# Kernel optimization log

Hardware: AMD Instinct MI355X
Metric: run time of the kernel (lower is better)

## Reference

```python
import jax, jax.numpy as jnp
import numpy as np

DIM=2048; NH=16; QK_NOPE=128; QK_ROPE=64; QK_HD=QK_NOPE+QK_ROPE; V_HD=128
Q_LORA=1536; KV_LORA=512
IDX_NH=16; IDX_HD=128; IDX_TOPK=1024
B=1; S=2048
NEG=-1e30  # finite stand-in for -inf mask

def _hadamard(n):
    H=np.array([[1.0]],dtype=np.float32)
    while H.shape[0]<n:
        H=np.block([[H,H],[H,-H]])
    return H
_H=jnp.asarray(_hadamard(IDX_HD),jnp.bfloat16)  # symmetric Sylvester Hadamard

def _rope_tables(s,d):
    inv=1.0/(10000.0**(np.arange(0,d,2)/float(d)))
    ang=np.outer(np.arange(s),inv)
    return jnp.asarray(np.cos(ang),jnp.float32),jnp.asarray(np.sin(ang),jnp.float32)

def _rope_interleaved(x,cos,sin):
    # pairs (x[2i], x[2i+1]); x: (b,s,h,d), cos/sin: (s,d//2)
    x1=x[...,0::2]; x2=x[...,1::2]
    c=cos[None,:,None,:]; s_=sin[None,:,None,:]
    return jnp.stack([x1*c-x2*s_,x1*s_+x2*c],axis=-1).reshape(x.shape)

def _rope_half(x,cos,sin):
    # non-interleaved: pairs (x[i], x[i+d/2])
    d=x.shape[-1]//2
    x1=x[...,:d]; x2=x[...,d:]
    c=cos[None,:,None,:]; s_=sin[None,:,None,:]
    return jnp.concatenate([x1*c-x2*s_,x1*s_+x2*c],axis=-1)

def _rms(x,w,eps=1e-6):
    xf=x.astype(jnp.float32)
    xf=xf*jax.lax.rsqrt(jnp.mean(xf*xf,axis=-1,keepdims=True)+eps)
    return (w*xf).astype(x.dtype)

def _ln(x,w,b,eps=1e-6):
    xf=x.astype(jnp.float32)
    mu=jnp.mean(xf,axis=-1,keepdims=True)
    var=jnp.mean((xf-mu)**2,axis=-1,keepdims=True)
    return ((xf-mu)*jax.lax.rsqrt(var+eps)*w+b).astype(x.dtype)

def _rotate(x):
    # rotate_activation: bf16 Hadamard transform, x @ H * d^-0.5 (H symmetric)
    return (x.astype(jnp.bfloat16)@_H)*(IDX_HD**-0.5)

def _forward(x,start_pos,freqs_cos,freqs_sin,mask,q_a_proj,q_a_ln_w,q_b_proj,kv_a_proj,kv_a_ln_w,kv_b_proj,o_proj,idx_wq_b,idx_wk,idx_knorm_w,idx_knorm_b,idx_weights_proj):
    b,s,_=x.shape  # start_pos==0 prefill -> cache slice == current k/kv
    sm_scale=QK_HD**-0.5
    qr=_rms(x@q_a_proj.T,q_a_ln_w)                       # (b,s,q_lora)
    q=(qr@q_b_proj.T).reshape(b,s,NH,QK_HD)
    q_nope=q[...,:QK_NOPE]
    q_pe=_rope_interleaved(q[...,QK_NOPE:],freqs_cos,freqs_sin)
    kvp=x@kv_a_proj.T
    kv=_rms(kvp[...,:KV_LORA],kv_a_ln_w)                 # latent kv cache (b,t,c)
    k_pe=_rope_interleaved(kvp[...,KV_LORA:][:,:,None,:],freqs_cos,freqs_sin)[:,:,0,:]
    # ---------- Indexer ----------
    iq=(qr@idx_wq_b.T).reshape(b,s,IDX_NH,IDX_HD)
    iq=jnp.concatenate([_rope_half(iq[...,:QK_ROPE],freqs_cos,freqs_sin),iq[...,QK_ROPE:]],axis=-1)
    ik=_ln(x@idx_wk.T,idx_knorm_w,idx_knorm_b)           # (b,s,IDX_HD)
    ik=jnp.concatenate([_rope_half(ik[:,:,None,:QK_ROPE],freqs_cos,freqs_sin)[:,:,0,:],ik[...,QK_ROPE:]],axis=-1)
    iq=_rotate(iq); ik=_rotate(ik)                       # bf16 Hadamard-rotated
    iw=(x@idx_weights_proj.T)*(IDX_NH**-0.5)             # (b,s,hI)
    wq=(iw[...,None]*iq.astype(jnp.float32)*(IDX_HD**-0.5)).astype(jnp.bfloat16)
    sc=jnp.einsum('bshd,btd->bsht',wq,ik,preferred_element_type=jnp.float32)
    index_score=jax.nn.relu(sc).sum(axis=2)+mask[None]   # bf16_index: relu, head-sum
    _,topk=jax.lax.top_k(index_score,min(IDX_TOPK,s))    # (b,s,K)
    imask=jnp.full((b,s,s),jnp.float32(NEG))
    imask=imask.at[jnp.arange(b)[:,None,None],jnp.arange(s)[None,:,None],topk].set(0.0)
    imask=imask+mask[None]
    # ---------- Latent attention (absorbed) ----------
    wkv=kv_b_proj.reshape(NH,QK_NOPE+V_HD,KV_LORA)
    q_abs=jnp.einsum('bshd,hdc->bshc',q_nope,wkv[:,:QK_NOPE])
    scores=(jnp.einsum('bshc,btc->bsht',q_abs,kv)+jnp.einsum('bshr,btr->bsht',q_pe,k_pe))*sm_scale
    scores=scores+imask[:,:,None,:]
    p=jax.nn.softmax(scores.astype(jnp.float32),axis=-1).astype(x.dtype)
    o=jnp.einsum('bsht,btc->bshc',p,kv)
    o=jnp.einsum('bshc,hdc->bshd',o,wkv[:,QK_NOPE:])
    return o.reshape(b,s,NH*V_HD)@o_proj.T

def setup_inputs():
    key=jax.random.key(0)
    ks=jax.random.split(key,10)
    def w(k,shape):
        return jax.random.normal(k,shape,jnp.float32)*(shape[-1]**-0.5)
    cos,sin=_rope_tables(S,QK_ROPE)
    causal=jnp.where(jnp.triu(jnp.ones((S,S),bool),1),jnp.float32(NEG),jnp.float32(0.0))
    return {
        'x':jax.random.normal(ks[0],(B,S,DIM),jnp.float32),
        'start_pos':0,
        'freqs_cos':cos,'freqs_sin':sin,'mask':causal,
        'q_a_proj':w(ks[1],(Q_LORA,DIM)),
        'q_a_ln_w':jnp.ones((Q_LORA,),jnp.float32),
        'q_b_proj':w(ks[2],(NH*QK_HD,Q_LORA)),
        'kv_a_proj':w(ks[3],(KV_LORA+QK_ROPE,DIM)),
        'kv_a_ln_w':jnp.ones((KV_LORA,),jnp.float32),
        'kv_b_proj':w(ks[4],(NH*(QK_NOPE+V_HD),KV_LORA)),
        'o_proj':w(ks[5],(DIM,NH*V_HD)),
        'idx_wq_b':w(ks[6],(IDX_NH*IDX_HD,Q_LORA)),
        'idx_wk':w(ks[7],(IDX_HD,DIM)),
        'idx_knorm_w':jnp.ones((IDX_HD,),jnp.float32),
        'idx_knorm_b':jnp.zeros((IDX_HD,),jnp.float32),
        'idx_weights_proj':w(ks[8],(IDX_NH,DIM)),
    }

def reference(x,start_pos,freqs_cos,freqs_sin,mask,q_a_proj,q_a_ln_w,q_b_proj,kv_a_proj,kv_a_ln_w,kv_b_proj,o_proj,idx_wq_b,idx_wk,idx_knorm_w,idx_knorm_b,idx_weights_proj):
    return _forward(x,start_pos,freqs_cos,freqs_sin,mask,q_a_proj,q_a_ln_w,q_b_proj,kv_a_proj,kv_a_ln_w,kv_b_proj,o_proj,idx_wq_b,idx_wk,idx_knorm_w,idx_knorm_b,idx_weights_proj)
```

## Files before the change

### kernel.cpp

```cpp
#include <hip/hip_runtime.h>
#include <hip/hip_bf16.h>
#include <math.h>

#define S 2048
#define NH 16
#define DIM 2048
#define QK_NOPE 128
#define QK_ROPE 64
#define QK_HD 192
#define V_HD 128
#define Q_LORA 1536
#define KV_LORA 512
#define IDX_HD 128
#define SM_SCALE 0.07216878364870323f
#define SCHUNK 512
#define PADK 40
#define XPLD 2256
#define QLD 5120
#define XPLD_PAD 2304

typedef __hip_bfloat16 bf16;
typedef unsigned short ushort_t;
typedef __attribute__((ext_vector_type(8))) short short8;
typedef __attribute__((ext_vector_type(4))) float f32x4;

__device__ __forceinline__ f32x4 mfma_bf16(short8 a, short8 b, f32x4 c) {
    return __builtin_amdgcn_mfma_f32_16x16x32_bf16(a, b, c, 0, 0, 0);
}
__device__ __forceinline__ void async16(const void* g, void* l) {
    __builtin_amdgcn_global_load_lds((const __attribute__((address_space(1))) void*)g,
                                     (__attribute__((address_space(3))) void*)l, 16, 0, 0);
}
__device__ __forceinline__ unsigned short f2bf(float f) {
    unsigned int u = __float_as_uint(f);
    return (unsigned short)((u + 0x7fff + ((u >> 16) & 1)) >> 16);
}
__device__ __forceinline__ float bf2f(unsigned short b) {
    return __uint_as_float(((unsigned int)b) << 16);
}

__global__ __launch_bounds__(256) void split_kernel(const float* __restrict__ in, ushort_t* __restrict__ hi,
                                                    ushort_t* __restrict__ lo, int n4) {
    int idx = blockIdx.x * 256 + threadIdx.x;
    if (idx >= n4) return;
    float4 v = ((const float4*)in)[idx];
    ushort4 h, l;
    h.x = f2bf(v.x); l.x = f2bf(v.x - bf2f(h.x));
    h.y = f2bf(v.y); l.y = f2bf(v.y - bf2f(h.y));
    h.z = f2bf(v.z); l.z = f2bf(v.z - bf2f(h.z));
    h.w = f2bf(v.w); l.w = f2bf(v.w - bf2f(h.w));
    ((ushort4*)hi)[idx] = h;
    ((ushort4*)lo)[idx] = l;
}

__global__ __launch_bounds__(256) void splitw2_kernel(const float* __restrict__ kv_b,
                                                      ushort_t* __restrict__ w2h, ushort_t* __restrict__ w2l) {
    int idx = blockIdx.x * 256 + threadIdx.x;
    int h = idx >> 14, rem = idx & 16383;
    int row = rem >> 7, c4 = (rem & 127) * 4;
    float4 v = *(const float4*)(kv_b + ((size_t)(h * 256 + 128 + row)) * 512 + c4);
    ushort4 hh, ll;
    hh.x = f2bf(v.x); ll.x = f2bf(v.x - bf2f(hh.x));
    hh.y = f2bf(v.y); ll.y = f2bf(v.y - bf2f(hh.y));
    hh.z = f2bf(v.z); ll.z = f2bf(v.z - bf2f(hh.z));
    hh.w = f2bf(v.w); ll.w = f2bf(v.w - bf2f(hh.w));
    *(ushort4*)(w2h + ((size_t)(h * 128 + row)) * 512 + c4) = hh;
    *(ushort4*)(w2l + ((size_t)(h * 128 + row)) * 512 + c4) = ll;
}

__global__ __launch_bounds__(256) void gemm3_lds(const ushort_t* __restrict__ Ah, const ushort_t* __restrict__ Al,
                                                 const ushort_t* __restrict__ Bh, const ushort_t* __restrict__ Bl,
                                                 float* __restrict__ C, int M, int N, int K) {
    __shared__ ushort_t sAh[128 * 32], sAl[128 * 32], sBh[128 * 32], sBl[128 * 32];
    const int tid = threadIdx.x;
    const int bm = blockIdx.y * 128, bn = blockIdx.x * 128;
    const int w = tid >> 6, lane = tid & 63;
    const int wm = (w >> 1) * 64, wn = (w & 1) * 64;
    const int fr = lane & 15, fk = (lane >> 4) * 8;
    const int srow = tid >> 2, skc = (tid & 3) * 8;
    f32x4 acc[4][4];
    for (int i = 0; i < 4; ++i)
        for (int j = 0; j < 4; ++j) acc[i][j] = f32x4{0.f, 0.f, 0.f, 0.f};
    const ushort_t* pAh0 = Ah + (size_t)(bm + srow) * K + skc;
    const ushort_t* pAh1 = Ah + (size_t)(bm + 64 + srow) * K + skc;
    const ushort_t* pAl0 = Al + (size_t)(bm + srow) * K + skc;
    const ushort_t* pAl1 = Al + (size_t)(bm + 64 + srow) * K + skc;
    const ushort_t* pBh0 = Bh + (size_t)(bn + srow) * K + skc;
    const ushort_t* pBh1 = Bh + (size_t)(bn + 64 + srow) * K + skc;
    const ushort_t* pBl0 = Bl + (size_t)(bn + srow) * K + skc;
    const ushort_t* pBl1 = Bl + (size_t)(bn + 64 + srow) * K + skc;
    ushort_t* dA0 = &sAh[srow * 32 + skc];
    ushort_t* dA1 = &sAh[(64 + srow) * 32 + skc];
    ushort_t* dAl0 = &sAl[srow * 32 + skc];
    ushort_t* dAl1 = &sAl[(64 + srow) * 32 + skc];
    ushort_t* dB0 = &sBh[srow * 32 + skc];
    ushort_t* dB1 = &sBh[(64 + srow) * 32 + skc];
    ushort_t* dBl0 = &sBl[srow * 32 + skc];
    ushort_t* dBl1 = &sBl[(64 + srow) * 32 + skc];
    for (int k0 = 0; k0 < K; k0 += 32) {
        __syncthreads();
        async16(pAh0, dA0);  async16(pAh1, dA1);
        async16(pAl0, dAl0); async16(pAl1, dAl1);
        async16(pBh0, dB0);  async16(pBh1, dB1);
        async16(pBl0, dBl0); async16(pBl1, dBl1);
        pAh0 += 32; pAh1 += 32; pAl0 += 32; pAl1 += 32;
        pBh0 += 32; pBh1 += 32; pBl0 += 32; pBl1 += 32;
        __syncthreads();
        short8 ahf[4], alf[4], bhf[4], blf[4];
        for (int i = 0; i < 4; ++i) {
            int ro = (wm + i * 16 + fr) * 32 + fk;
            ahf[i] = *(const short8*)&sAh[ro];
            alf[i] = *(const short8*)&sAl[ro];
        }
        for (int j = 0; j < 4; ++j) {
            int ro = (wn + j * 16 + fr) * 32 + fk;
            bhf[j] = *(const short8*)&sBh[ro];
            blf[j] = *(const short8*)&sBl[ro];
        }
        for (int i = 0; i < 4; ++i)
            for (int j = 0; j < 4; ++j) {
                acc[i][j] = mfma_bf16(ahf[i], bhf[j], acc[i][j]);
                acc[i][j] = mfma_bf16(ahf[i], blf[j], acc[i][j]);
                acc[i][j] = mfma_bf16(alf[i], bhf[j], acc[i][j]);
            }
    }
    const int cr = (lane >> 4) * 4, cc = lane & 15;
    for (int i = 0; i < 4; ++i)
        for (int j = 0; j < 4; ++j) {
            int row = bm + wm + i * 16 + cr;
            int col = bn + wn + j * 16 + cc;
            if (col < N)
                for (int r = 0; r < 4; ++r)
                    C[(size_t)(row + r) * N + col] = acc[i][j][r];
        }
}

__global__ __launch_bounds__(256) void rms_kernel(const float* __restrict__ in, float* __restrict__ out,
                                                  const float* __restrict__ w, int C, int ldin, int ldout) {
    const int row = blockIdx.x;
    const float* xr = in + (size_t)row * ldin;
    float* yr = out + (size_t)row * ldout;
    float ss = 0.f;
    for (int c = threadIdx.x; c < C; c += 256) { float v = xr[c]; ss += v * v; }
    for (int o = 32; o; o >>= 1) ss += __shfl_down(ss, o, 64);
    __shared__ float red[4];
    const int wave = threadIdx.x >> 6, lane = threadIdx.x & 63;
    if (lane == 0) red[wave] = ss;
    __syncthreads();
    const float tot = red[0] + red[1] + red[2] + red[3];
    const float scale = rsqrtf(tot / (float)C + 1e-6f);
    for (int c = threadIdx.x; c < C; c += 256) yr[c] = w[c] * (xr[c] * scale);
}

__global__ __launch_bounds__(256) void rms_split_kernel(const float* __restrict__ in, ushort_t* __restrict__ hi,
                                                        ushort_t* __restrict__ lo, const float* __restrict__ w,
                                                        int C, int ldin) {
    const int row = blockIdx.x;
    const float* xr = in + (size_t)row * ldin;
    float ss = 0.f;
    for (int c = threadIdx.x; c < C; c += 256) { float v = xr[c]; ss += v * v; }
    for (int o = 32; o; o >>= 1) ss += __shfl_down(ss, o, 64);
    __shared__ float red[4];
    const int wave = threadIdx.x >> 6, lane = threadIdx.x & 63;
    if (lane == 0) red[wave] = ss;
    __syncthreads();
    const float tot = red[0] + red[1] + red[2] + red[3];
    const float scale = rsqrtf(tot / (float)C + 1e-6f);
    for (int c = threadIdx.x; c < C; c += 256) {
        float v = w[c] * (xr[c] * scale);
        unsigned short h = f2bf(v);
        hi[(size_t)row * C + c] = h;
        lo[(size_t)row * C + c] = f2bf(v - bf2f(h));
    }
}

__global__ __launch_bounds__(128) void ln_kernel(float* __restrict__ x, const float* __restrict__ w,
                                                 const float* __restrict__ b, int ld) {
    const int row = blockIdx.x;
    float* xr = x + (size_t)row * ld;
    const int tid = threadIdx.x;
    float v = xr[tid];
    float sm = v;
    for (int o = 32; o; o >>= 1) sm += __shfl_down(sm, o, 64);
    __shared__ float red[2];
    if ((tid & 63) == 0) red[tid >> 6] = sm;
    __syncthreads();
    const float mu = (red[0] + red[1]) * (1.f / 128.f);
    __syncthreads();
    float d = v - mu;
    float sv = d * d;
    for (int o = 32; o; o >>= 1) sv += __shfl_down(sv, o, 64);
    if ((tid & 63) == 0) red[tid >> 6] = sv;
    __syncthreads();
    const float var = (red[0] + red[1]) * (1.f / 128.f);
    const float rs = rsqrtf(var + 1e-6f);
    xr[tid] = (v - mu) * rs * w[tid] + b[tid];
}

__global__ __launch_bounds__(256) void rope_inter_kernel(float* __restrict__ X, const float* __restrict__ ct,
                                                         const float* __restrict__ st, int H, int hs, int off,
                                                         int ld) {
    int idx = blockIdx.x * 256 + threadIdx.x;
    int k = idx & 31;
    int h = (idx >> 5) % H;
    int s = idx / (32 * H);
    if (s >= S) return;
    float c = ct[s * 32 + k], sn = st[s * 32 + k];
    float* p = X + (size_t)s * ld + h * hs + off;
    float x1 = p[2 * k], x2 = p[2 * k + 1];
    p[2 * k]     = x1 * c - x2 * sn;
    p[2 * k + 1] = x1 * sn + x2 * c;
}

__global__ __launch_bounds__(256) void rope_half_kernel(float* __restrict__ X, const float* __restrict__ ct,
                                                        const float* __restrict__ st, int H, int hs, int ld) {
    int idx = blockIdx.x * 256 + threadIdx.x;
    int k = idx & 31;
    int h = (idx >> 5) % H;
    int s = idx / (32 * H);
    if (s >= S) return;
    float c = ct[s * 32 + k], sn = st[s * 32 + k];
    float* p = X + (size_t)s * ld + h * hs;
    float x1 = p[k], x2 = p[32 + k];
    p[k]      = x1 * c - x2 * sn;
    p[32 + k] = x1 * sn + x2 * c;
}

__global__ __launch_bounds__(128) void rotate_kernel(const float* __restrict__ in, int lds, int H,
                                                     bf16* __restrict__ out) {
    __shared__ float xs[128];
    const int r = blockIdx.x, j = threadIdx.x;
    const int s = r / H, h = r - s * H;
    float v = in[(size_t)s * lds + h * 128 + j];
    xs[j] = __bfloat162float(__float2bfloat16(v));
    __syncthreads();
    float acc = 0.f;
    for (int d = 0; d < 128; ++d) {
        float xv = xs[d];
        acc += (__popc(d & j) & 1) ? -xv : xv;
    }
    float t = __bfloat162float(__float2bfloat16(acc)) * 0.08838834764831845f;
    out[(size_t)r * 128 + j] = __float2bfloat16(t);
}

__global__ __launch_bounds__(256) void wq_kernel(const float* __restrict__ iwb, bf16* __restrict__ iqr) {
    int idx = blockIdx.x * 256 + threadIdx.x;
    int s = idx >> 11, h = (idx >> 7) & 15;
    float a = 0.25f * iwb[(size_t)s * XPLD + h];
    float v = __bfloat162float(iqr[idx]);
    float t = (a * v) * 0.08838834764831845f;
    iqr[idx] = __float2bfloat16(t);
}

__global__ __launch_bounds__(256) void iscore_mfma(const bf16* __restrict__ wq, const bf16* __restrict__ ik,
                                                   float* __restrict__ out) {
    if (blockIdx.x > blockIdx.y) return;
    __shared__ unsigned short As[128 * 32], Bs[128 * 32];
    const int bs = blockIdx.y * 128, bt = blockIdx.x * 128;
    const int tid = threadIdx.x, w = tid >> 6, lane = tid & 63;
    const int wm = (w >> 1) * 64, wn = (w & 1) * 64;
    const int fr = lane & 15, fk = (lane >> 4) * 8;
    const int srow = lane >> 2, skc = (lane & 3) * 8;
    f32x4 sum[4][4];
    for (int i = 0; i < 4; ++i)
        for (int j = 0; j < 4; ++j) sum[i][j] = f32x4{0.f, 0.f, 0.f, 0.f};
    for (int h = 0; h < 16; ++h) {
        f32x4 acc[4][4];
        for (int i = 0; i < 4; ++i)
            for (int j = 0; j < 4; ++j) acc[i][j] = f32x4{0.f, 0.f, 0.f, 0.f};
        for (int k0 = 0; k0 < 128; k0 += 32) {
            __syncthreads();
            for (int i = 0; i < 2; ++i) {
                int seg = i * 4 + w;
                async16(wq + (size_t)(bs + seg * 16 + srow) * 2048 + h * 128 + k0 + skc, &As[seg * 512]);
                async16(ik + (size_t)(bt + seg * 16 + srow) * 128 + k0 + skc, &Bs[seg * 512]);
            }
            __syncthreads();
            short8 af[4], bff[4];
            for (int i = 0; i < 4; ++i) af[i]  = *(const short8*)&As[(wm + i * 16 + fr) * 32 + fk];
            for (int j = 0; j < 4; ++j) bff[j] = *(const short8*)&Bs[(wn + j * 16 + fr) * 32 + fk];
            for (int i = 0; i < 4; ++i)
                for (int j = 0; j < 4; ++j)
                    acc[i][j] = mfma_bf16(af[i], bff[j], acc[i][j]);
        }
        for (int i = 0; i < 4; ++i)
            for (int j = 0; j < 4; ++j)
                for (int r = 0; r < 4; ++r)
                    sum[i][j][r] += fmaxf(acc[i][j][r], 0.f);
    }
    const int cr = (lane >> 4) * 4, cc = lane & 15;
    for (int i = 0; i < 4; ++i)
        for (int j = 0; j < 4; ++j)
            for (int r = 0; r < 4; ++r)
                out[(size_t)(bs + wm + i * 16 + cr + r) * 2048 + bt + wn + j * 16 + cc] = sum[i][j][r];
}

__global__ __launch_bounds__(256) void topk_kernel(const float* __restrict__ isc, int* __restrict__ tk) {
    __shared__ unsigned long long keys[2048];
    const int s = blockIdx.x;
    const float* row = isc + (size_t)s * 2048;
    for (int t = threadIdx.x; t < 2048; t += 256) {
        unsigned long long kk = 0ull;
        if (t <= s) {
            unsigned int vb = __float_as_uint(row[t]);
            kk = ((unsigned long long)vb << 32) | (unsigned int)(2048 - t);
        }
        keys[t] = kk;
    }
    __syncthreads();
    for (int k = 2; k <= 2048; k <<= 1) {
        for (int j = k >> 1; j > 0; j >>= 1) {
            for (int t = threadIdx.x; t < 2048; t += 256) {
                int l = t ^ j;
                if (l > t) {
                    bool up = ((t & k) == 0);
                    unsigned long long a = keys[t], b = keys[l];
                    bool sw = up ? (a < b) : (a > b);
                    if (sw) { keys[t] = b; keys[l] = a; }
                }
            }
            __syncthreads();
        }
    }
    const int cnt = min(1024, s + 1);
    for (int i = threadIdx.x; i < 1024; i += 256) {
        int t = (i < cnt) ? (2048 - (int)(keys[i] & 0xFFFFFFFFull)) : -1;
        tk[(size_t)s * 1024 + i] = t;
    }
}

__global__ __launch_bounds__(256) void w1t_kernel(const float* __restrict__ kv_b, float* __restrict__ w1t) {
    __shared__ float ts[64][65];
    const int cb = blockIdx.x * 64, db = blockIdx.y * 64, h = blockIdx.z;
    const int t = threadIdx.x;
    for (int it = 0; it < 16; ++it) {
        int idx = it * 256 + t;
        int rr = idx >> 6, cc = idx & 63;
        ts[rr][cc] = kv_b[(size_t)(h * 256 + db + rr) * 512 + cb + cc];
    }
    __syncthreads();
    for (int it = 0; it < 16; ++it) {
        int idx = it * 256 + t;
        int rr = idx >> 6, cc = idx & 63;
        w1t[(size_t)h * 65536 + (size_t)(cb + rr) * 128 + db + cc] = ts[cc][rr];
    }
}

__global__ __launch_bounds__(576) void kvsplit_kernel(const float* __restrict__ kv, const float* __restrict__ kpe,
                                                      ushort_t* __restrict__ kvh, ushort_t* __restrict__ kvl,
                                                      unsigned int* __restrict__ kvi) {
    const int t = blockIdx.x, c = threadIdx.x;
    float v = (c < 512) ? kv[(size_t)t * 512 + c] : kpe[(size_t)t * XPLD + c];
    unsigned short hi = f2bf(v);
    unsigned short lo = f2bf(v - bf2f(hi));
    kvh[(size_t)t * 576 + c] = hi;
    kvl[(size_t)t * 576 + c] = lo;
    if (c < 512) kvi[(size_t)t * 512 + c] = (unsigned int)hi | ((unsigned int)lo << 16);
}

__global__ __launch_bounds__(256) void qabs_mfma(const float* __restrict__ q, const float* __restrict__ w1t,
                                                 ushort_t* __restrict__ qah, ushort_t* __restrict__ qal) {
    __shared__ unsigned short Ah[128 * PADK], Al[128 * PADK], Bh[128 * PADK], Bl[128 * PADK];
    const int tid = threadIdx.x;
    const int bn = blockIdx.x * 128, bm = blockIdx.y * 128, h = blockIdx.z;
    const int w = tid >> 6, lane = tid & 63;
    const int wm = (w >> 1) * 64, wn = (w & 1) * 64;
    const int fr = lane & 15, fk = (lane >> 4) * 8;
    f32x4 acc[4][4];
    for (int i = 0; i < 4; ++i)
        for (int j = 0; j < 4; ++j) acc[i][j] = f32x4{0.f, 0.f, 0.f, 0.f};
    for (int k0 = 0; k0 < 128; k0 += 32) {
        __syncthreads();
        for (int it = 0; it < 4; ++it) {
            int f = it * 256 + tid;
            int row = f >> 3, kc = (f & 7) * 4;
            float4 av = *(const float4*)(q + (size_t)(bm + row) * QLD + h * QK_HD + k0 + kc);
            float4 bv = *(const float4*)(w1t + (size_t)h * 65536 + (size_t)(bn + row) * 128 + k0 + kc);
            ushort4 ahi, alo, bhi, blo;
            ahi.x = f2bf(av.x); alo.x = f2bf(av.x - bf2f(ahi.x));
            ahi.y = f2bf(av.y); alo.y = f2bf(av.y - bf2f(ahi.y));
            ahi.z = f2bf(av.z); alo.z = f2bf(av.z - bf2f(ahi.z));
            ahi.w = f2bf(av.w); alo.w = f2bf(av.w - bf2f(ahi.w));
            bhi.x = f2bf(bv.x); blo.x = f2bf(bv.x - bf2f(bhi.x));
            bhi.y = f2bf(bv.y); blo.y = f2bf(bv.y - bf2f(bhi.y));
            bhi.z = f2bf(bv.z); blo.z = f2bf(bv.z - bf2f(bhi.z));
            bhi.w = f2bf(bv.w); blo.w = f2bf(bv.w - bf2f(bhi.w));
            *(ushort4*)&Ah[row * PADK + kc] = ahi;
            *(ushort4*)&Al[row * PADK + kc] = alo;
            *(ushort4*)&Bh[row * PADK + kc] = bhi;
            *(ushort4*)&Bl[row * PADK + kc] = blo;
        }
        __syncthreads();
        short8 ahf[4], alf[4], bhf[4], blf[4];
        for (int i = 0; i < 4; ++i) {
            int ro = (wm + i * 16 + fr) * PADK + fk;
            ahf[i] = *(const short8*)&Ah[ro];
            alf[i] = *(const short8*)&Al[ro];
        }
        for (int j = 0; j < 4; ++j) {
            int ro = (wn + j * 16 + fr) * PADK + fk;
            bhf[j] = *(const short8*)&Bh[ro];
            blf[j] = *(const short8*)&Bl[ro];
        }
        for (int i = 0; i < 4; ++i)
            for (int j = 0; j < 4; ++j) {
                acc[i][j] = mfma_bf16(ahf[i], bhf[j], acc[i][j]);
                acc[i][j] = mfma_bf16(ahf[i], blf[j], acc[i][j]);
                acc[i][j] = mfma_bf16(alf[i], bhf[j], acc[i][j]);
            }
    }
    const int cr = (lane >> 4) * 4, cc = lane & 15;
    for (int i = 0; i < 4; ++i)
        for (int j = 0; j < 4; ++j)
            for (int r = 0; r < 4; ++r) {
                int srow = bm + wm + i * 16 + cr + r;
                int col = bn + wn + j * 16 + cc;
                float f = acc[i][j][r] * SM_SCALE;
                size_t addr = ((size_t)srow * 16 + h) * 576 + col;
                unsigned short hi = f2bf(f);
                qah[addr] = hi;
                qal[addr] = f2bf(f - bf2f(hi));
            }
}

__global__ __launch_bounds__(256) void qpe_split(const float* __restrict__ q, ushort_t* __restrict__ qah,
                                                 ushort_t* __restrict__ qal) {
    int idx = blockIdx.x * 256 + threadIdx.x;
    int r = idx & 63, h = (idx >> 6) & 15, s = idx >> 10;
    float f = q[(size_t)s * QLD + h * QK_HD + 128 + r] * SM_SCALE;
    size_t addr = ((size_t)s * 16 + h) * 576 + 512 + r;
    unsigned short hi = f2bf(f);
    qah[addr] = hi;
    qal[addr] = f2bf(f - bf2f(hi));
}

__global__ __launch_bounds__(512) void attn_score_mfma(const ushort_t* __restrict__ qah,
                                                       const ushort_t* __restrict__ qal,
                                                       const ushort_t* __restrict__ kvh,
                                                       const ushort_t* __restrict__ kvl,
                                                       const int* __restrict__ tk,
                                                       float* __restrict__ scb, int s0) {
    const int sl = blockIdx.x, s = s0 + sl, pass = blockIdx.y;
    const int tid = threadIdx.x, w = tid >> 6, lane = tid & 63;
    const int cnt = min(1024, s + 1);
    if (pass * 256 >= cnt) {
        for (int i = tid; i < 4096; i += 512) {
            int head = i >> 8, key = i & 255;
            scb[((size_t)sl * 16 + head) * 1024 + pass * 256 + key] = -1e30f;
        }
        return;
    }
    __shared__ int tks[256];
    __shared__ __align__(16) ushort_t kh[2][8192], kl[2][8192];
    if (tid < 256) {
        int t = tk[(size_t)s * 1024 + pass * 256 + tid];
        tks[tid] = t < 0 ? 0 : t;
    }
    __syncthreads();
    const int fr = lane & 15, g = lane >> 4;
    const size_t abase = ((size_t)s * 16 + fr) * 576 + g * 8;
    const int R0 = tid >> 2;
    const int sw = (tid & 3) ^ ((R0 >> 1) & 3);
    const size_t t0 = (size_t)tks[R0], t1 = (size_t)tks[R0 + 128];
    const ushort_t* gh0 = kvh + t0 * 576 + sw * 8;
    const ushort_t* gh1 = kvh + t1 * 576 + sw * 8;
    const ushort_t* gl0 = kvl + t0 * 576 + sw * 8;
    const ushort_t* gl1 = kvl + t1 * 576 + sw * 8;
    const int ro_a = (w * 32 + fr) * 32 + ((g ^ ((fr >> 1) & 3)) << 3);
    async16(gh0, &kh[0][w * 512]);
    async16(gh1, &kh[0][4096 + w * 512]);
    async16(gl0, &kl[0][w * 512]);
    async16(gl1, &kl[0][4096 + w * 512]);
    short8 qh = *(const short8*)(qah + abase);
    short8 ql = *(const short8*)(qal + abase);
    f32x4 acc0 = {0.f, 0.f, 0.f, 0.f}, acc1 = {0.f, 0.f, 0.f, 0.f};
    int cur = 0;
    __syncthreads();
    for (int ch = 0; ch < 18; ++ch) {
        if (ch < 17) {
            int off = (ch + 1) * 32;
            async16(gh0 + off, &kh[cur ^ 1][w * 512]);
            async16(gh1 + off, &kh[cur ^ 1][4096 + w * 512]);
            async16(gl0 + off, &kl[cur ^ 1][w * 512]);
            async16(gl1 + off, &kl[cur ^ 1][4096 + w * 512]);
        }
        short8 qhc = qh, qlc = ql;
        if (ch < 17) {
            qh = *(const short8*)(qah + abase + (ch + 1) * 32);
            ql = *(const short8*)(qal + abase + (ch + 1) * 32);
        }
        short8 bh0 = *(const short8*)&kh[cur][ro_a];
        short8 bl0 = *(const short8*)&kl[cur][ro_a];
        short8 bh1 = *(const short8*)&kh[cur][ro_a + 512];
        short8 bl1 = *(const short8*)&kl[cur][ro_a + 512];
        acc0 = mfma_bf16(qhc, bh0, acc0);
        acc0 = mfma_bf16(qhc, bl0, acc0);
        acc0 = mfma_bf16(qlc, bh0, acc0);
        acc1 = mfma_bf16(qhc, bh1, acc1);
        acc1 = mfma_bf16(qhc, bl1, acc1);
        acc1 = mfma_bf16(qlc, bh1, acc1);
        __syncthreads();
        cur ^= 1;
    }
    const int cr = (lane >> 4) * 4, cc = lane & 15;
    for (int r = 0; r < 4; ++r) {
        int head = cr + r;
        int key0 = pass * 256 + w * 32 + cc;
        int key1 = key0 + 16;
        scb[((size_t)sl * 16 + head) * 1024 + key0] = (key0 < cnt) ? acc0[r] : -1e30f;
        scb[((size_t)sl * 16 + head) * 1024 + key1] = (key1 < cnt) ? acc1[r] : -1e30f;
    }
}

__global__ __launch_bounds__(256) void softmax_pb(const float* __restrict__ scb,
                                                  ushort_t* __restrict__ pbh, ushort_t* __restrict__ pbl) {
    const size_t row = blockIdx.x;
    const float* src = scb + row * 1024;
    const int tid = threadIdx.x, wave = tid >> 6, lane = tid & 63;
    __shared__ float red[4];
    float v[4];
    float m = -INFINITY;
    for (int i = 0; i < 4; ++i) { v[i] = src[tid + 256 * i]; m = fmaxf(m, v[i]); }
    for (int o = 32; o; o >>= 1) m = fmaxf(m, __shfl_down(m, o, 64));
    if (lane == 0) red[wave] = m;
    __syncthreads();
    m = fmaxf(fmaxf(red[0], red[1]), fmaxf(red[2], red[3]));
    __syncthreads();
    float e[4], l = 0.f;
    for (int i = 0; i < 4; ++i) { e[i] = __expf(v[i] - m); l += e[i]; }
    for (int o = 32; o; o >>= 1) l += __shfl_down(l, o, 64);
    if (lane == 0) red[wave] = l;
    __syncthreads();
    const float il = 1.f / (red[0] + red[1] + red[2] + red[3]);
    for (int i = 0; i < 4; ++i) {
        float p = e[i] * il;
        unsigned short hi = f2bf(p);
        pbh[row * 1024 + tid + 256 * i] = hi;
        pbl[row * 1024 + tid + 256 * i] = f2bf(p - bf2f(hi));
    }
}

#define PV_GATHER(KC)                                                                    \
    g0 = *(const uint4*)(kvi + (size_t)tks[(KC) * 32 + r0     ] * 512 + gp4);            \
    g1 = *(const uint4*)(kvi + (size_t)tks[(KC) * 32 + r0 + 4 ] * 512 + gp4);            \
    g2 = *(const uint4*)(kvi + (size_t)tks[(KC) * 32 + r0 + 8 ] * 512 + gp4);            \
    g3 = *(const uint4*)(kvi + (size_t)tks[(KC) * 32 + r0 + 12] * 512 + gp4);            \
    g4 = *(const uint4*)(kvi + (size_t)tks[(KC) * 32 + r0 + 16] * 512 + gp4);            \
    g5 = *(const uint4*)(kvi + (size_t)tks[(KC) * 32 + r0 + 20] * 512 + gp4);            \
    g6 = *(const uint4*)(kvi + (size_t)tks[(KC) * 32 + r0 + 24] * 512 + gp4);            \
    g7 = *(const uint4*)(kvi + (size_t)tks[(KC) * 32 + r0 + 28] * 512 + gp4);
#define PV_STORE()                                                                       \
    *(uint4*)&vt[(r0     ) * 512 + ((gp ^ 0) << 2)] = g0;                                \
    *(uint4*)&vt[(r0 + 4 ) * 512 + ((gp ^ 0) << 2)] = g1;                                \
    *(uint4*)&vt[(r0 + 8 ) * 512 + ((gp ^ 2) << 2)] = g2;                                \
    *(uint4*)&vt[(r0 + 12) * 512 + ((gp ^ 2) << 2)] = g3;                                \
    *(uint4*)&vt[(r0 + 16) * 512 + ((gp ^ 4) << 2)] = g4;                                \
    *(uint4*)&vt[(r0 + 20) * 512 + ((gp ^ 4) << 2)] = g5;                                \
    *(uint4*)&vt[(r0 + 24) * 512 + ((gp ^ 6) << 2)] = g6;                                \
    *(uint4*)&vt[(r0 + 28) * 512 + ((gp ^ 6) << 2)] = g7;
__global__ __launch_bounds__(512) void attn_pv_mfma(const ushort_t* __restrict__ pbh,
                                                    const ushort_t* __restrict__ pbl,
                                                    const unsigned int* __restrict__ kvi,
                                                    const int* __restrict__ tk,
                                                    ushort_t* __restrict__ o1h, ushort_t* __restrict__ o1l,
                                                    int s0) {
    const int sl = blockIdx.x, s = s0 + sl;
    const int tid = threadIdx.x, w = tid >> 6, lane = tid & 63;
    __shared__ int tks[1024];
    __shared__ unsigned int vt[32 * 512];
    for (int j = tid; j < 1024; j += 512) {
        int t = tk[(size_t)s * 1024 + j];
        tks[j] = t < 0 ? 0 : t;
    }
    const int fr = lane & 15, g = lane >> 4, fko = g * 8;
    const int r0 = tid >> 7;
    const int gp = tid & 127;
    const int gp4 = gp * 4;
    f32x4 acc[4];
    for (int i = 0; i < 4; ++i) acc[i] = f32x4{0.f, 0.f, 0.f, 0.f};
    const size_t pbase = ((size_t)sl * 16 + fr) * 1024 + fko;
    uint4 g0, g1, g2, g3, g4, g5, g6, g7;
    __syncthreads();
    PV_GATHER(0)
    PV_STORE()
    __syncthreads();
    for (int kc = 0; kc < 32; ++kc) {
        if (kc < 31) {
            PV_GATHER(kc + 1)
        }
        short8 ph = *(const short8*)(pbh + pbase + kc * 32);
        short8 pl = *(const short8*)(pbl + pbase + kc * 32);
        #pragma unroll
        for (int sub = 0; sub < 4; ++sub) {
            const int cb = (w * 64 + sub * 16 + fr) ^ (g << 3);
            short8 bh, bl;
            #pragma unroll
            for (int jj = 0; jj < 8; ++jj) {
                const unsigned int v = vt[(fko + jj) * 512 + cb];
                bh[jj] = (short)(v & 0xffffu);
                bl[jj] = (short)(v >> 16);
            }
            acc[sub] = mfma_bf16(ph, bh, acc[sub]);
            acc[sub] = mfma_bf16(pl, bh, acc[sub]);
            acc[sub] = mfma_bf16(ph, bl, acc[sub]);
        }
        __syncthreads();
        if (kc < 31) {
            PV_STORE()
            __syncthreads();
        }
    }
    const int cr = (lane >> 4) * 4, cc = lane & 15;
    for (int sub = 0; sub < 4; ++sub)
        for (int r = 0; r < 4; ++r) {
            int head = cr + r, c = w * 64 + sub * 16 + cc;
            float f = acc[sub][r];
            unsigned short hv = f2bf(f);
            size_t addr = ((size_t)sl * 16 + head) * 512 + c;
            o1h[addr] = hv;
            o1l[addr] = f2bf(f - bf2f(hv));
        }
}

__global__ __launch_bounds__(256) void outproj_mfma(const ushort_t* __restrict__ o1h,
                                                    const ushort_t* __restrict__ o1l,
                                                    const ushort_t* __restrict__ w2h,
                                                    const ushort_t* __restrict__ w2l,
                                                    ushort_t* __restrict__ o2h, ushort_t* __restrict__ o2l,
                                                    int s0) {
    __shared__ ushort_t sAh[128 * 32], sAl[128 * 32], sBh[128 * 32], sBl[128 * 32];
    const int tid = threadIdx.x;
    const int bm = blockIdx.x * 128, h = blockIdx.y;
    const int w = tid >> 6, lane = tid & 63;
    const int wm = (w >> 1) * 64, wn = (w & 1) * 64;
    const int fr = lane & 15, fk = (lane >> 4) * 8;
    const int srow = tid >> 2, skc = (tid & 3) * 8;
    f32x4 acc[4][4];
    for (int i = 0; i < 4; ++i)
        for (int j = 0; j < 4; ++j) acc[i][j] = f32x4{0.f, 0.f, 0.f, 0.f};
    const ushort_t* pAh0 = o1h + ((size_t)(bm + srow) * 16 + h) * 512 + skc;
    const ushort_t* pAh1 = o1h + ((size_t)(bm + 64 + srow) * 16 + h) * 512 + skc;
    const ushort_t* pAl0 = o1l + ((size_t)(bm + srow) * 16 + h) * 512 + skc;
    const ushort_t* pAl1 = o1l + ((size_t)(bm + 64 + srow) * 16 + h) * 512 + skc;
    const ushort_t* pBh0 = w2h + ((size_t)(h * 128 + srow)) * 512 + skc;
    const ushort_t* pBh1 = w2h + ((size_t)(h * 128 + 64 + srow)) * 512 + skc;
    const ushort_t* pBl0 = w2l + ((size_t)(h * 128 + srow)) * 512 + skc;
    const ushort_t* pBl1 = w2l + ((size_t)(h * 128 + 64 + srow)) * 512 + skc;
    ushort_t* dA0 = &sAh[srow * 32 + skc];
    ushort_t* dA1 = &sAh[(64 + srow) * 32 + skc];
    ushort_t* dAl0 = &sAl[srow * 32 + skc];
    ushort_t* dAl1 = &sAl[(64 + srow) * 32 + skc];
    ushort_t* dB0 = &sBh[srow * 32 + skc];
    ushort_t* dB1 = &sBh[(64 + srow) * 32 + skc];
    ushort_t* dBl0 = &sBl[srow * 32 + skc];
    ushort_t* dBl1 = &sBl[(64 + srow) * 32 + skc];
    for (int k0 = 0; k0 < 512; k0 += 32) {
        __syncthreads();
        async16(pAh0, dA0);  async16(pAh1, dA1);
        async16(pAl0, dAl0); async16(pAl1, dAl1);
        async16(pBh0, dB0);  async16(pBh1, dB1);
        async16(pBl0, dBl0); async16(pBl1, dBl1);
        pAh0 += 32; pAh1 += 32; pAl0 += 32; pAl1 += 32;
        pBh0 += 32; pBh1 += 32; pBl0 += 32; pBl1 += 32;
        __syncthreads();
        short8 ahf[4], alf[4], bhf[4], blf[4];
        for (int i = 0; i < 4; ++i) {
            int ro = (wm + i * 16 + fr) * 32 + fk;
            ahf[i] = *(const short8*)&sAh[ro];
            alf[i] = *(const short8*)&sAl[ro];
        }
        for (int j = 0; j < 4; ++j) {
            int ro = (wn + j * 16 + fr) * 32 + fk;
            bhf[j] = *(const short8*)&sBh[ro];
            blf[j] = *(const short8*)&sBl[ro];
        }
        for (int i = 0; i < 4; ++i)
            for (int j = 0; j < 4; ++j) {
                acc[i][j] = mfma_bf16(ahf[i], bhf[j], acc[i][j]);
                acc[i][j] = mfma_bf16(ahf[i], blf[j], acc[i][j]);
                acc[i][j] = mfma_bf16(alf[i], bhf[j], acc[i][j]);
            }
    }
    const int cr = (lane >> 4) * 4, cc = lane & 15;
    for (int i = 0; i < 4; ++i)
        for (int j = 0; j < 4; ++j)
            for (int r = 0; r < 4; ++r) {
                int srow2 = s0 + bm + wm + i * 16 + cr + r;
                int col = wn + j * 16 + cc;
                size_t addr = (size_t)srow2 * 2048 + h * 128 + col;
                float f = acc[i][j][r];
                unsigned short hv = f2bf(f);
                o2h[addr] = hv;
                o2l[addr] = f2bf(f - bf2f(hv));
            }
}

extern "C" void kernel_launch(void* const* d_in, const int* in_sizes, int n_in,
                              void* d_out, int out_size, void* d_ws, size_t ws_size,
                              hipStream_t stream) {
    const float* x         = (const float*)d_in[0];
    const float* fcos      = (const float*)d_in[2];
    const float* fsin      = (const float*)d_in[3];
    const float* q_a_proj  = (const float*)d_in[5];
    const float* q_a_ln_w  = (const float*)d_in[6];
    const float* q_b_proj  = (const float*)d_in[7];
    const float* kv_a_proj = (const float*)d_in[8];
    const float* kv_a_ln_w = (const float*)d_in[9];
    const float* kv_b      = (const float*)d_in[10];
    const float* o_proj    = (const float*)d_in[11];
    const float* idx_wq_b  = (const float*)d_in[12];
    const float* idx_wk    = (const float*)d_in[13];
    const float* iknw      = (const float*)d_in[14];
    const float* iknb      = (const float*)d_in[15];
    const float* idx_wp    = (const float*)d_in[16];
    float* out = (float*)d_out;

    char* ws = (char*)d_ws;
    size_t off = 0;
    auto alloc = [&](size_t bytes) {
        char* p = ws + off;
        off += (bytes + 255) & ~(size_t)255;
        return p;
    };
    float* xp  = (float*)alloc((size_t)S * XPLD * 4);
    ushort_t* qrh = (ushort_t*)alloc((size_t)S * Q_LORA * 2);
    ushort_t* qrl = (ushort_t*)alloc((size_t)S * Q_LORA * 2);
    float* qib = (float*)alloc((size_t)S * QLD * 4);
    char* RAt  = alloc(31457280);
    float* isc = (float*)RAt;
    bf16* iqr  = (bf16*)(RAt + 16777216);
    bf16* ikr  = (bf16*)(RAt + 16777216 + 8388608);
    ushort_t* xh = (ushort_t*)RAt;
    ushort_t* xl = xh + (size_t)S * DIM;
    ushort_t* wq2h = (ushort_t*)RAt;
    ushort_t* wq2l = wq2h + (size_t)5120 * Q_LORA;
    float* w1t = (float*)RAt;
    ushort_t* wpackh = (ushort_t*)qib;
    ushort_t* wpackl = wpackh + (size_t)XPLD_PAD * DIM;
    char* kvtail = RAt + (size_t)22 * 1024 * 1024;
    unsigned int* kvi = (unsigned int*)kvtail;
    ushort_t* w2h = (ushort_t*)(kvtail + (size_t)4 * 1024 * 1024);
    ushort_t* w2l = w2h + (size_t)16 * 128 * 512;
    const size_t CHUNK_BYTES = (size_t)SCHUNK * 16 * 1024 * 4 + (size_t)SCHUNK * 16 * 1024 * 2 * 2
                             + (size_t)SCHUNK * 16 * 512 * 4;
    if (off < CHUNK_BYTES) off = (CHUNK_BYTES + 255) & ~(size_t)255;
    int* tk        = (int*)alloc((size_t)S * 1024 * 4);
    float* kv      = (float*)alloc((size_t)S * KV_LORA * 4);
    ushort_t* o2h  = (ushort_t*)alloc((size_t)S * 2048 * 2);
    ushort_t* o2l  = (ushort_t*)alloc((size_t)S * 2048 * 2);
    ushort_t* qah  = (ushort_t*)alloc((size_t)S * 16 * 576 * 2);
    ushort_t* qal  = (ushort_t*)alloc((size_t)S * 16 * 576 * 2);
    ushort_t* kvh  = (ushort_t*)alloc((size_t)S * 576 * 2);
    ushort_t* kvl  = (ushort_t*)alloc((size_t)S * 576 * 2);
    float* scb    = (float*)ws;
    ushort_t* pbh = (ushort_t*)(ws + (size_t)SCHUNK * 16 * 1024 * 4);
    ushort_t* pbl = pbh + (size_t)SCHUNK * 16 * 1024;
    ushort_t* o1h = (ushort_t*)(ws + (size_t)SCHUNK * 16 * 1024 * 8);
    ushort_t* o1l = o1h + (size_t)SCHUNK * 16 * 512;
    ushort_t* oph = (ushort_t*)ws;
    ushort_t* opl = oph + (size_t)DIM * 2048;

    split_kernel<<<S * DIM / 1024, 256, 0, stream>>>(x, xh, xl, S * DIM / 4);
    split_kernel<<<Q_LORA * DIM / 1024, 256, 0, stream>>>(q_a_proj, wpackh, wpackl, Q_LORA * DIM / 4);
    split_kernel<<<576 * DIM / 1024, 256, 0, stream>>>(kv_a_proj, wpackh + (size_t)1536 * DIM,
                                                       wpackl + (size_t)1536 * DIM, 576 * DIM / 4);
    split_kernel<<<128 * DIM / 1024, 256, 0, stream>>>(idx_wk, wpackh + (size_t)2112 * DIM,
                                                       wpackl + (size_t)2112 * DIM, 128 * DIM / 4);
    split_kernel<<<16 * DIM / 1024, 256, 0, stream>>>(idx_wp, wpackh + (size_t)2240 * DIM,
                                                      wpackl + (size_t)2240 * DIM, 16 * DIM / 4);
    hipMemsetAsync(wpackh + (size_t)XPLD * DIM, 0, (size_t)(XPLD_PAD - XPLD) * DIM * 2, stream);
    hipMemsetAsync(wpackl + (size_t)XPLD * DIM, 0, (size_t)(XPLD_PAD - XPLD) * DIM * 2, stream);
    gemm3_lds<<<dim3((XPLD + 127) / 128, S / 128), 256, 0, stream>>>(xh, xl, wpackh, wpackl, xp, S, XPLD, DIM);
    rms_split_kernel<<<S, 256, 0, stream>>>(xp, qrh, qrl, q_a_ln_w, Q_LORA, XPLD);
    rms_kernel<<<S, 256, 0, stream>>>(xp + 1536, kv, kv_a_ln_w, KV_LORA, XPLD, KV_LORA);
    split_kernel<<<3072 * Q_LORA / 1024, 256, 0, stream>>>(q_b_proj, wq2h, wq2l, 3072 * Q_LORA / 4);
    split_kernel<<<2048 * Q_LORA / 1024, 256, 0, stream>>>(idx_wq_b, wq2h + (size_t)3072 * Q_LORA,
                                                           wq2l + (size_t)3072 * Q_LORA, 2048 * Q_LORA / 4);
    gemm3_lds<<<dim3(QLD / 128, S / 128), 256, 0, stream>>>(qrh, qrl, wq2h, wq2l, qib, S, QLD, Q_LORA);
    rope_inter_kernel<<<S * NH * 32 / 256, 256, 0, stream>>>(qib, fcos, fsin, NH, QK_HD, QK_NOPE, QLD);
    rope_inter_kernel<<<S * 32 / 256, 256, 0, stream>>>(xp + 1536, fcos, fsin, 1, 0, KV_LORA, XPLD);
    rope_half_kernel<<<S * NH * 32 / 256, 256, 0, stream>>>(qib + 3072, fcos, fsin, NH, 128, QLD);
    ln_kernel<<<S, 128, 0, stream>>>(xp + 2112, iknw, iknb, XPLD);
    rope_half_kernel<<<S * 32 / 256, 256, 0, stream>>>(xp + 2112, fcos, fsin, 1, 0, XPLD);
    rotate_kernel<<<S * NH, 128, 0, stream>>>(qib + 3072, QLD, NH, iqr);
    rotate_kernel<<<S, 128, 0, stream>>>(xp + 2112, XPLD, 1, ikr);
    wq_kernel<<<S * NH * 128 / 256, 256, 0, stream>>>(xp + 2240, iqr);
    iscore_mfma<<<dim3(16, 16), 256, 0, stream>>>(iqr, ikr, isc);
    topk_kernel<<<S, 256, 0, stream>>>(isc, tk);
    w1t_kernel<<<dim3(8, 2, 16), 256, 0, stream>>>(kv_b, w1t);
    qabs_mfma<<<dim3(4, S / 128, 16), 256, 0, stream>>>(qib, w1t, qah, qal);
    qpe_split<<<S * NH * 64 / 256, 256, 0, stream>>>(qib, qah, qal);
    kvsplit_kernel<<<S, 576, 0, stream>>>(kv, xp + 1536, kvh, kvl, kvi);
    splitw2_kernel<<<1024, 256, 0, stream>>>(kv_b, w2h, w2l);
    for (int c = 0; c < 4; ++c) {
        int s0 = c * SCHUNK;
        attn_score_mfma<<<dim3(SCHUNK, 4), 512, 0, stream>>>(qah, qal, kvh, kvl, tk, scb, s0);
        softmax_pb<<<SCHUNK * 16, 256, 0, stream>>>(scb, pbh, pbl);
        attn_pv_mfma<<<SCHUNK, 512, 0, stream>>>(pbh, pbl, kvi, tk, o1h, o1l, s0);
        outproj_mfma<<<dim3(4, 16), 256, 0, stream>>>(o1h, o1l, w2h, w2l, o2h, o2l, s0);
    }
    split_kernel<<<DIM * 2048 / 1024, 256, 0, stream>>>(o_proj, oph, opl, DIM * 2048 / 4);
    gemm3_lds<<<dim3(DIM / 128, S / 128), 256, 0, stream>>>(o2h, o2l, oph, opl, out, S, DIM, NH * V_HD);
}
```

Measured before the change: 1.590 ms.

## Skip indexer work for the first 1024 rows where top-k selects all keys

For query rows with s < 1024 the causal top-1024 selection covers every valid key, so the indexer pipeline (rope, rotate, weighting, score GEMM, top-k sort) now runs only for rows 1024 and up. The attention score and PV kernels gain a dense flag that uses identity key indices for the first two chunks instead of reading the top-k table. This removes roughly half the indexer compute and the per-row bitonic sort. It relies on the ordering of selected keys not mattering, which holds since softmax and PV are order-invariant.

```diff
diff --git a/kernel.cpp b/kernel.cpp
--- a/kernel.cpp
+++ b/kernel.cpp
@@ -213,11 +213,12 @@
 }
 
 __global__ __launch_bounds__(256) void rope_half_kernel(float* __restrict__ X, const float* __restrict__ ct,
-                                                        const float* __restrict__ st, int H, int hs, int ld) {
+                                                        const float* __restrict__ st, int H, int hs, int ld,
+                                                        int soff) {
     int idx = blockIdx.x * 256 + threadIdx.x;
     int k = idx & 31;
     int h = (idx >> 5) % H;
-    int s = idx / (32 * H);
+    int s = idx / (32 * H) + soff;
     if (s >= S) return;
     float c = ct[s * 32 + k], sn = st[s * 32 + k];
     float* p = X + (size_t)s * ld + h * hs;
@@ -227,9 +228,9 @@
 }
 
 __global__ __launch_bounds__(128) void rotate_kernel(const float* __restrict__ in, int lds, int H,
-                                                     bf16* __restrict__ out) {
+                                                     bf16* __restrict__ out, int roff) {
     __shared__ float xs[128];
-    const int r = blockIdx.x, j = threadIdx.x;
+    const int r = blockIdx.x + roff, j = threadIdx.x;
     const int s = r / H, h = r - s * H;
     float v = in[(size_t)s * lds + h * 128 + j];
     xs[j] = __bfloat162float(__float2bfloat16(v));
@@ -243,8 +244,9 @@
     out[(size_t)r * 128 + j] = __float2bfloat16(t);
 }
 
-__global__ __launch_bounds__(256) void wq_kernel(const float* __restrict__ iwb, bf16* __restrict__ iqr) {
-    int idx = blockIdx.x * 256 + threadIdx.x;
+__global__ __launch_bounds__(256) void wq_kernel(const float* __restrict__ iwb, bf16* __restrict__ iqr,
+                                                 int ioff) {
+    int idx = blockIdx.x * 256 + threadIdx.x + ioff;
     int s = idx >> 11, h = (idx >> 7) & 15;
     float a = 0.25f * iwb[(size_t)s * XPLD + h];
     float v = __bfloat162float(iqr[idx]);
@@ -254,9 +256,9 @@
 
 __global__ __launch_bounds__(256) void iscore_mfma(const bf16* __restrict__ wq, const bf16* __restrict__ ik,
                                                    float* __restrict__ out) {
-    if (blockIdx.x > blockIdx.y) return;
+    if (blockIdx.x > blockIdx.y + 8) return;
     __shared__ unsigned short As[128 * 32], Bs[128 * 32];
-    const int bs = blockIdx.y * 128, bt = blockIdx.x * 128;
+    const int bs = (blockIdx.y + 8) * 128, bt = blockIdx.x * 128;
     const int tid = threadIdx.x, w = tid >> 6, lane = tid & 63;
     const int wm = (w >> 1) * 64, wn = (w & 1) * 64;
     const int fr = lane & 15, fk = (lane >> 4) * 8;
@@ -295,9 +297,10 @@
                 out[(size_t)(bs + wm + i * 16 + cr + r) * 2048 + bt + wn + j * 16 + cc] = sum[i][j][r];
 }
 
-__global__ __launch_bounds__(256) void topk_kernel(const float* __restrict__ isc, int* __restrict__ tk) {
+__global__ __launch_bounds__(256) void topk_kernel(const float* __restrict__ isc, int* __restrict__ tk,
+                                                   int s0) {
     __shared__ unsigned long long keys[2048];
-    const int s = blockIdx.x;
+    const int s = s0 + blockIdx.x;
     const float* row = isc + (size_t)s * 2048;
     for (int t = threadIdx.x; t < 2048; t += 256) {
         unsigned long long kk = 0ull;
@@ -439,7 +442,7 @@
                                                        const ushort_t* __restrict__ kvh,
                                                        const ushort_t* __restrict__ kvl,
                                                        const int* __restrict__ tk,
-                                                       float* __restrict__ scb, int s0) {
+                                                       float* __restrict__ scb, int s0, int dense) {
     const int sl = blockIdx.x, s = s0 + sl, pass = blockIdx.y;
     const int tid = threadIdx.x, w = tid >> 6, lane = tid & 63;
     const int cnt = min(1024, s + 1);
@@ -453,8 +456,12 @@
     __shared__ int tks[256];
     __shared__ __align__(16) ushort_t kh[2][8192], kl[2][8192];
     if (tid < 256) {
-        int t = tk[(size_t)s * 1024 + pass * 256 + tid];
-        tks[tid] = t < 0 ? 0 : t;
+        if (dense) {
+            tks[tid] = pass * 256 + tid;
+        } else {
+            int t = tk[(size_t)s * 1024 + pass * 256 + tid];
+            tks[tid] = t < 0 ? 0 : t;
+        }
     }
     __syncthreads();
     const int fr = lane & 15, g = lane >> 4;
@@ -563,14 +570,18 @@
                                                     const unsigned int* __restrict__ kvi,
                                                     const int* __restrict__ tk,
                                                     ushort_t* __restrict__ o1h, ushort_t* __restrict__ o1l,
-                                                    int s0) {
+                                                    int s0, int dense) {
     const int sl = blockIdx.x, s = s0 + sl;
     const int tid = threadIdx.x, w = tid >> 6, lane = tid & 63;
     __shared__ int tks[1024];
     __shared__ unsigned int vt[32 * 512];
     for (int j = tid; j < 1024; j += 512) {
-        int t = tk[(size_t)s * 1024 + j];
-        tks[j] = t < 0 ? 0 : t;
+        if (dense) {
+            tks[j] = j;
+        } else {
+            int t = tk[(size_t)s * 1024 + j];
+            tks[j] = t < 0 ? 0 : t;
+        }
     }
     const int fr = lane & 15, g = lane >> 4, fko = g * 8;
     const int r0 = tid >> 7;
@@ -779,14 +790,14 @@
     gemm3_lds<<<dim3(QLD / 128, S / 128), 256, 0, stream>>>(qrh, qrl, wq2h, wq2l, qib, S, QLD, Q_LORA);
     rope_inter_kernel<<<S * NH * 32 / 256, 256, 0, stream>>>(qib, fcos, fsin, NH, QK_HD, QK_NOPE, QLD);
     rope_inter_kernel<<<S * 32 / 256, 256, 0, stream>>>(xp + 1536, fcos, fsin, 1, 0, KV_LORA, XPLD);
-    rope_half_kernel<<<S * NH * 32 / 256, 256, 0, stream>>>(qib + 3072, fcos, fsin, NH, 128, QLD);
+    rope_half_kernel<<<S * NH * 32 / 512, 256, 0, stream>>>(qib + 3072, fcos, fsin, NH, 128, QLD, 1024);
     ln_kernel<<<S, 128, 0, stream>>>(xp + 2112, iknw, iknb, XPLD);
-    rope_half_kernel<<<S * 32 / 256, 256, 0, stream>>>(xp + 2112, fcos, fsin, 1, 0, XPLD);
-    rotate_kernel<<<S * NH, 128, 0, stream>>>(qib + 3072, QLD, NH, iqr);
-    rotate_kernel<<<S, 128, 0, stream>>>(xp + 2112, XPLD, 1, ikr);
-    wq_kernel<<<S * NH * 128 / 256, 256, 0, stream>>>(xp + 2240, iqr);
-    iscore_mfma<<<dim3(16, 16), 256, 0, stream>>>(iqr, ikr, isc);
-    topk_kernel<<<S, 256, 0, stream>>>(isc, tk);
+    rope_half_kernel<<<S * 32 / 256, 256, 0, stream>>>(xp + 2112, fcos, fsin, 1, 0, XPLD, 0);
+    rotate_kernel<<<S * NH / 2, 128, 0, stream>>>(qib + 3072, QLD, NH, iqr, 1024 * NH);
+    rotate_kernel<<<S, 128, 0, stream>>>(xp + 2112, XPLD, 1, ikr, 0);
+    wq_kernel<<<S * NH * 128 / 512, 256, 0, stream>>>(xp + 2240, iqr, 1024 * NH * 128);
+    iscore_mfma<<<dim3(16, 8), 256, 0, stream>>>(iqr, ikr, isc);
+    topk_kernel<<<1024, 256, 0, stream>>>(isc, tk, 1024);
     w1t_kernel<<<dim3(8, 2, 16), 256, 0, stream>>>(kv_b, w1t);
     qabs_mfma<<<dim3(4, S / 128, 16), 256, 0, stream>>>(qib, w1t, qah, qal);
     qpe_split<<<S * NH * 64 / 256, 256, 0, stream>>>(qib, qah, qal);
@@ -794,9 +805,10 @@
     splitw2_kernel<<<1024, 256, 0, stream>>>(kv_b, w2h, w2l);
     for (int c = 0; c < 4; ++c) {
         int s0 = c * SCHUNK;
-        attn_score_mfma<<<dim3(SCHUNK, 4), 512, 0, stream>>>(qah, qal, kvh, kvl, tk, scb, s0);
+        int dense = (c < 2) ? 1 : 0;
+        attn_score_mfma<<<dim3(SCHUNK, 4), 512, 0, stream>>>(qah, qal, kvh, kvl, tk, scb, s0, dense);
         softmax_pb<<<SCHUNK * 16, 256, 0, stream>>>(scb, pbh, pbl);
-        attn_pv_mfma<<<SCHUNK, 512, 0, stream>>>(pbh, pbl, kvi, tk, o1h, o1l, s0);
+        attn_pv_mfma<<<SCHUNK, 512, 0, stream>>>(pbh, pbl, kvi, tk, o1h, o1l, s0, dense);
         outproj_mfma<<<dim3(4, 16), 256, 0, stream>>>(o1h, o1l, w2h, w2l, o2h, o2l, s0);
     }
     split_kernel<<<DIM * 2048 / 1024, 256, 0, stream>>>(o_proj, oph, opl, DIM * 2048 / 4);
```

New measurement: 1.515 ms. -4.7%, faster.
